# Kernel optimization log

Hardware: AMD Instinct MI355X
Metric: run time of the kernel (lower is better)

The kernel has to match this reference:

```python
import jax, jax.numpy as jnp
import numpy as np

N_SEG = 1024  # segments per image (ids are contiguous in [0, N_SEG) after reindex_batch_segments)


def setup_inputs() -> dict:
    key = jax.random.key(0)
    k1, k2, k3, k4 = jax.random.split(key, 4)
    B, C, Hf, Wf = 4, 256, 16, 16
    H, W = 512, 512
    F_out = 192
    features = jax.random.normal(k1, (B, C, Hf, Wf), dtype=jnp.float32)
    w_conv = jax.random.normal(k2, (F_out, C), dtype=jnp.float32) / np.sqrt(C)
    b_conv = jax.random.normal(k3, (F_out,), dtype=jnp.float32) * 0.01
    segment = jax.random.randint(k4, (B, H, W), 0, N_SEG, dtype=jnp.int32)
    return {"features": features, "w_conv": w_conv, "b_conv": b_conv, "segment": segment}


def reference(features, w_conv, b_conv, segment):
    # features: (B, C, Hf, Wf) backbone output; segment: (B, H, W) int ids in [0, N_SEG)
    B, C, Hf, Wf = features.shape
    _, H, W = segment.shape
    # F.interpolate(..., mode='bilinear', align_corners=False) == half-pixel linear resize
    up = jax.image.resize(features, (B, C, H, W), method="bilinear")
    pix = up.transpose(0, 2, 3, 1).reshape(B * H * W, C)  # (B*H*W, C)
    # offset per-image segment ids into a global id space: id + b * N_SEG
    seg = (segment.reshape(B, H * W) + (jnp.arange(B, dtype=segment.dtype) * N_SEG)[:, None]).reshape(-1)
    sums = jax.ops.segment_sum(pix, seg, num_segments=B * N_SEG)              # (B*N, C)
    cnt = jax.ops.segment_sum(jnp.ones((B * H * W,), pix.dtype), seg, num_segments=B * N_SEG)
    mean = sums / jnp.maximum(cnt, 1.0)[:, None]
    feats = mean.reshape(B, N_SEG, C)                                          # (B, N, C)
    # last_conv: 1x1 Conv1d (C -> F_out) applied on (B, C, N), then permute(0, 2, 1)
    out = jnp.einsum("bnc,fc->bnf", feats, w_conv) + b_conv                    # (B, N, F_out)
    return out, segment
```

## Files before the change

### kernel.cpp

```cpp
#include <hip/hip_runtime.h>
#include <hip/hip_bf16.h>

constexpr int B_   = 4;
constexpr int C_   = 256;
constexpr int HF   = 16;
constexpr int WF   = 16;
constexpr int HH   = 512;
constexpr int WW   = 512;
constexpr int NSEG = 1024;
constexpr int FOUT = 192;
constexpr int NCELL = HF * WF;
constexpr int CB    = B_ * NCELL;
constexpr int GPB   = 48;

struct PS { float Fs[32][65]; float Ws[64][33]; };

union CellSMem {
    struct { unsigned lbin[NSEG]; unsigned wc[64]; } c;
    PS p;
};

__device__ void gemm_P_body(int gp, const float* __restrict__ feat,
                            const float* __restrict__ w, float* __restrict__ P,
                            PS& sm) {
    int ni = gp % 3;
    int mi = (gp / 3) & 3;
    int b  = gp / 12;
    const float* Fb = feat + (size_t)b * C_ * NCELL;

    int tid = threadIdx.x;
    int tx = tid & 15, ty = tid >> 4;
    float acc[4][4] = {};

    for (int k0 = 0; k0 < C_; k0 += 32) {
        #pragma unroll
        for (int l = 0; l < 2; ++l) {
            int li = tid * 2 + l;
            int kk = li >> 4;
            int m4 = (li & 15) * 4;
            float4 vf = *reinterpret_cast<const float4*>(&Fb[(size_t)(k0 + kk) * NCELL + mi * 64 + m4]);
            sm.Fs[kk][m4 + 0] = vf.x; sm.Fs[kk][m4 + 1] = vf.y;
            sm.Fs[kk][m4 + 2] = vf.z; sm.Fs[kk][m4 + 3] = vf.w;
            int row = li >> 3;
            int kq  = (li & 7) * 4;
            float4 vw = *reinterpret_cast<const float4*>(&w[(size_t)(ni * 64 + row) * C_ + k0 + kq]);
            sm.Ws[row][kq + 0] = vw.x; sm.Ws[row][kq + 1] = vw.y;
            sm.Ws[row][kq + 2] = vw.z; sm.Ws[row][kq + 3] = vw.w;
        }
        __syncthreads();
        #pragma unroll
        for (int kk = 0; kk < 32; ++kk) {
            float ar[4], wr[4];
            #pragma unroll
            for (int i = 0; i < 4; ++i) ar[i] = sm.Fs[kk][ty * 4 + i];
            #pragma unroll
            for (int j = 0; j < 4; ++j) wr[j] = sm.Ws[tx * 4 + j][kk];
            #pragma unroll
            for (int i = 0; i < 4; ++i)
                #pragma unroll
                for (int j = 0; j < 4; ++j) acc[i][j] += ar[i] * wr[j];
        }
        __syncthreads();
    }

    #pragma unroll
    for (int i = 0; i < 4; ++i)
        #pragma unroll
        for (int j = 0; j < 4; ++j)
            P[(size_t)b * NCELL * FOUT + (size_t)(mi * 64 + ty * 4 + i) * FOUT + ni * 64 + tx * 4 + j] = acc[i][j];
}

__device__ __forceinline__ unsigned tapw(int v, int cc) {
    if (v < 0 || v >= 512) return 0u;
    int twov = 2 * v - 31;
    int num  = ((twov % 64) + 64) % 64;
    int iv   = (twov - num) >> 6;
    int v0 = max(iv, 0), v1 = min(iv + 1, 15);
    return (unsigned)((v0 == cc ? 64 - num : 0) + (v1 == cc ? num : 0));
}

__global__ __launch_bounds__(256) void k_cell(const int* __restrict__ seg,
                                              float* __restrict__ segout,
                                              float* __restrict__ AT,
                                              const float* __restrict__ feat,
                                              const float* __restrict__ w,
                                              float* __restrict__ P) {
    __shared__ CellSMem sm;
    int blk = blockIdx.x;
    if (blk < GPB) { gemm_P_body(blk, feat, w, P, sm.p); return; }

    int cb   = blk - GPB;
    int tid  = threadIdx.x;
    int b    = cb >> 8;
    int cell = cb & 255;
    int cy = cell >> 4, cx = cell & 15;
    int ys = 32 * cy - 16, xs = 32 * cx - 16;

    const int4* sv = reinterpret_cast<const int4*>(seg + (size_t)cb * 1024);
    float4*     ov = reinterpret_cast<float4*>(segout + (size_t)cb * 1024);
    int4 pv = sv[tid];

    #pragma unroll
    for (int j = 0; j < 4; ++j) sm.c.lbin[tid * 4 + j] = 0u;
    if (tid < 64) sm.c.wc[tid] = tapw(xs + tid, cx);

    int r  = tid >> 2;
    int y  = ys + r;
    unsigned wrv = tapw(y, cy);
    int yc = min(max(y, 0), HH - 1);
    int cg = (tid & 3) * 16;
    int x0 = xs + cg;
    int xc = min(max(x0, 0), WW - 16);

    const int4* lrow = reinterpret_cast<const int4*>(seg + (size_t)b * (HH * WW) + (size_t)yc * WW + xc);
    int4 v0 = lrow[0], v1 = lrow[1], v2 = lrow[2], v3 = lrow[3];

    ov[tid] = make_float4((float)pv.x, (float)pv.y, (float)pv.z, (float)pv.w);
    __syncthreads();

    uint4 wa = *reinterpret_cast<const uint4*>(&sm.c.wc[cg + 0]);
    uint4 wb = *reinterpret_cast<const uint4*>(&sm.c.wc[cg + 4]);
    uint4 wcv = *reinterpret_cast<const uint4*>(&sm.c.wc[cg + 8]);
    uint4 wd = *reinterpret_cast<const uint4*>(&sm.c.wc[cg + 12]);

    atomicAdd(&sm.c.lbin[v0.x], wrv * wa.x);
    atomicAdd(&sm.c.lbin[v0.y], wrv * wa.y);
    atomicAdd(&sm.c.lbin[v0.z], wrv * wa.z);
    atomicAdd(&sm.c.lbin[v0.w], wrv * wa.w);
    atomicAdd(&sm.c.lbin[v1.x], wrv * wb.x);
    atomicAdd(&sm.c.lbin[v1.y], wrv * wb.y);
    atomicAdd(&sm.c.lbin[v1.z], wrv * wb.z);
    atomicAdd(&sm.c.lbin[v1.w], wrv * wb.w);
    atomicAdd(&sm.c.lbin[v2.x], wrv * wcv.x);
    atomicAdd(&sm.c.lbin[v2.y], wrv * wcv.y);
    atomicAdd(&sm.c.lbin[v2.z], wrv * wcv.z);
    atomicAdd(&sm.c.lbin[v2.w], wrv * wcv.w);
    atomicAdd(&sm.c.lbin[v3.x], wrv * wd.x);
    atomicAdd(&sm.c.lbin[v3.y], wrv * wd.y);
    atomicAdd(&sm.c.lbin[v3.z], wrv * wd.z);
    atomicAdd(&sm.c.lbin[v3.w], wrv * wd.w);
    __syncthreads();

    float4* dst = reinterpret_cast<float4*>(AT + ((size_t)(b * NCELL + cell)) * NSEG);
    constexpr float SCL = 1.0f / 4096.0f;
    dst[tid] = make_float4(sm.c.lbin[tid * 4 + 0] * SCL, sm.c.lbin[tid * 4 + 1] * SCL,
                           sm.c.lbin[tid * 4 + 2] * SCL, sm.c.lbin[tid * 4 + 3] * SCL);
}

__global__ __launch_bounds__(256) void k_gemm_out(const float* __restrict__ AT,
                                                  const float* __restrict__ P,
                                                  const float* __restrict__ bias,
                                                  float* __restrict__ out) {
    int ft = blockIdx.x % 3;
    int st = blockIdx.x / 3;
    int b  = st >> 5;
    int s0 = (st & 31) * 32;

    const float* ATb = AT + (size_t)b * NCELL * NSEG;
    const float* Pb  = P  + (size_t)b * NCELL * FOUT;

    __shared__ float As[32][33];
    __shared__ float Ps[32][65];

    int tid = threadIdx.x;
    int tx = tid & 15, ty = tid >> 4;
    float acc[2][4] = {};
    float cnt[2] = {};

    for (int k0 = 0; k0 < NCELL; k0 += 32) {
        {
            int kk = tid >> 3, e4 = (tid & 7) * 4;
            float4 va = *reinterpret_cast<const float4*>(&ATb[(size_t)(k0 + kk) * NSEG + s0 + e4]);
            As[kk][e4 + 0] = va.x; As[kk][e4 + 1] = va.y;
            As[kk][e4 + 2] = va.z; As[kk][e4 + 3] = va.w;
            #pragma unroll
            for (int l = 0; l < 2; ++l) {
                int li = tid * 2 + l;
                int kp = li >> 4, e = (li & 15) * 4;
                float4 vp = *reinterpret_cast<const float4*>(&Pb[(size_t)(k0 + kp) * FOUT + ft * 64 + e]);
                Ps[kp][e + 0] = vp.x; Ps[kp][e + 1] = vp.y;
                Ps[kp][e + 2] = vp.z; Ps[kp][e + 3] = vp.w;
            }
        }
        __syncthreads();
        #pragma unroll
        for (int kk = 0; kk < 32; ++kk) {
            float ar[2], wr[4];
            #pragma unroll
            for (int i = 0; i < 2; ++i) { ar[i] = As[kk][ty * 2 + i]; cnt[i] += ar[i]; }
            #pragma unroll
            for (int j = 0; j < 4; ++j) wr[j] = Ps[kk][tx * 4 + j];
            #pragma unroll
            for (int i = 0; i < 2; ++i)
                #pragma unroll
                for (int j = 0; j < 4; ++j) acc[i][j] += ar[i] * wr[j];
        }
        __syncthreads();
    }

    #pragma unroll
    for (int i = 0; i < 2; ++i) {
        int row = b * NSEG + s0 + ty * 2 + i;
        float rinv = 1.0f / fmaxf(cnt[i], 1.0f);
        #pragma unroll
        for (int j = 0; j < 4; ++j) {
            int f = ft * 64 + tx * 4 + j;
            out[(size_t)row * FOUT + f] = acc[i][j] * rinv + bias[f];
        }
    }
}

extern "C" void kernel_launch(void* const* d_in, const int* in_sizes, int n_in,
                              void* d_out, int out_size, void* d_ws, size_t ws_size,
                              hipStream_t stream) {
    const float* feat = (const float*)d_in[0];
    const float* w    = (const float*)d_in[1];
    const float* bias = (const float*)d_in[2];
    const int*   seg  = (const int*)d_in[3];

    float* out    = (float*)d_out;
    float* segout = out + (size_t)B_ * NSEG * FOUT;

    char* wsb = (char*)d_ws;
    float* AT = (float*)wsb;
    float* P  = (float*)(wsb + (5u << 20));

    k_cell    <<<GPB + CB, 256, 0, stream>>>(seg, segout, AT, feat, w, P);
    k_gemm_out<<<(B_ * NSEG / 32) * (FOUT / 64), 256, 0, stream>>>(AT, P, bias, out);
}
```

Measured before the change: 48.54 us.

## Replace shared-memory tiled GEMMs with per-thread register-accumulating direct-load loops

Both small GEMMs (features x weights into P, and the per-segment weights AT x P into the output) drop their LDS tiling and __syncthreads. Each thread now computes one row times 16 output columns, streaming operands straight from global/L2 with broadcast loads of P and w. The output GEMM launches 192 blocks instead of 384 and writes float4 stores. This removes barrier and LDS staging overhead, but it lowers parallelism and relies on cache broadcast for operand reuse.

```diff
diff --git a/kernel.cpp b/kernel.cpp
--- a/kernel.cpp
+++ b/kernel.cpp
@@ -13,61 +13,30 @@
 constexpr int CB    = B_ * NCELL;
 constexpr int GPB   = 48;
 
-struct PS { float Fs[32][65]; float Ws[64][33]; };
+__device__ void gemm_P_body(int gp, const float* __restrict__ feat,
+                            const float* __restrict__ w, float* __restrict__ P) {
+    int b  = gp / 12;
+    int f0 = (gp % 12) * 16;
+    int ij = threadIdx.x;
+    const float* Fb = feat + (size_t)b * C_ * NCELL + ij;
 
-union CellSMem {
-    struct { unsigned lbin[NSEG]; unsigned wc[64]; } c;
-    PS p;
-};
-
-__device__ void gemm_P_body(int gp, const float* __restrict__ feat,
-                            const float* __restrict__ w, float* __restrict__ P,
-                            PS& sm) {
-    int ni = gp % 3;
-    int mi = (gp / 3) & 3;
-    int b  = gp / 12;
-    const float* Fb = feat + (size_t)b * C_ * NCELL;
-
-    int tid = threadIdx.x;
-    int tx = tid & 15, ty = tid >> 4;
-    float acc[4][4] = {};
-
-    for (int k0 = 0; k0 < C_; k0 += 32) {
+    float acc[16] = {};
+    for (int c0 = 0; c0 < C_; c0 += 4) {
+        float fv0 = Fb[(size_t)(c0 + 0) * NCELL];
+        float fv1 = Fb[(size_t)(c0 + 1) * NCELL];
+        float fv2 = Fb[(size_t)(c0 + 2) * NCELL];
+        float fv3 = Fb[(size_t)(c0 + 3) * NCELL];
         #pragma unroll
-        for (int l = 0; l < 2; ++l) {
-            int li = tid * 2 + l;
-            int kk = li >> 4;
-            int m4 = (li & 15) * 4;
-            float4 vf = *reinterpret_cast<const float4*>(&Fb[(size_t)(k0 + kk) * NCELL + mi * 64 + m4]);
-            sm.Fs[kk][m4 + 0] = vf.x; sm.Fs[kk][m4 + 1] = vf.y;
-            sm.Fs[kk][m4 + 2] = vf.z; sm.Fs[kk][m4 + 3] = vf.w;
-            int row = li >> 3;
-            int kq  = (li & 7) * 4;
-            float4 vw = *reinterpret_cast<const float4*>(&w[(size_t)(ni * 64 + row) * C_ + k0 + kq]);
-            sm.Ws[row][kq + 0] = vw.x; sm.Ws[row][kq + 1] = vw.y;
-            sm.Ws[row][kq + 2] = vw.z; sm.Ws[row][kq + 3] = vw.w;
+        for (int j = 0; j < 16; ++j) {
+            float4 wv = *reinterpret_cast<const float4*>(&w[(size_t)(f0 + j) * C_ + c0]);
+            acc[j] += fv0 * wv.x + fv1 * wv.y + fv2 * wv.z + fv3 * wv.w;
         }
-        __syncthreads();
-        #pragma unroll
-        for (int kk = 0; kk < 32; ++kk) {
-            float ar[4], wr[4];
-            #pragma unroll
-            for (int i = 0; i < 4; ++i) ar[i] = sm.Fs[kk][ty * 4 + i];
-            #pragma unroll
-            for (int j = 0; j < 4; ++j) wr[j] = sm.Ws[tx * 4 + j][kk];
-            #pragma unroll
-            for (int i = 0; i < 4; ++i)
-                #pragma unroll
-                for (int j = 0; j < 4; ++j) acc[i][j] += ar[i] * wr[j];
-        }
-        __syncthreads();
     }
-
+    float* Pp = P + (size_t)b * NCELL * FOUT + (size_t)ij * FOUT + f0;
     #pragma unroll
-    for (int i = 0; i < 4; ++i)
-        #pragma unroll
-        for (int j = 0; j < 4; ++j)
-            P[(size_t)b * NCELL * FOUT + (size_t)(mi * 64 + ty * 4 + i) * FOUT + ni * 64 + tx * 4 + j] = acc[i][j];
+    for (int j4 = 0; j4 < 4; ++j4)
+        *reinterpret_cast<float4*>(Pp + j4 * 4) =
+            make_float4(acc[j4 * 4 + 0], acc[j4 * 4 + 1], acc[j4 * 4 + 2], acc[j4 * 4 + 3]);
 }
 
 __device__ __forceinline__ unsigned tapw(int v, int cc) {
@@ -79,17 +48,11 @@
     return (unsigned)((v0 == cc ? 64 - num : 0) + (v1 == cc ? num : 0));
 }
 
-__global__ __launch_bounds__(256) void k_cell(const int* __restrict__ seg,
-                                              float* __restrict__ segout,
-                                              float* __restrict__ AT,
-                                              const float* __restrict__ feat,
-                                              const float* __restrict__ w,
-                                              float* __restrict__ P) {
-    __shared__ CellSMem sm;
-    int blk = blockIdx.x;
-    if (blk < GPB) { gemm_P_body(blk, feat, w, P, sm.p); return; }
+struct CS { unsigned lbin[NSEG]; unsigned wc[64]; };
 
-    int cb   = blk - GPB;
+__device__ void cell_body(int cb, const int* __restrict__ seg,
+                          float* __restrict__ segout, float* __restrict__ AT,
+                          CS& sm) {
     int tid  = threadIdx.x;
     int b    = cb >> 8;
     int cell = cb & 255;
@@ -101,8 +64,8 @@
     int4 pv = sv[tid];
 
     #pragma unroll
-    for (int j = 0; j < 4; ++j) sm.c.lbin[tid * 4 + j] = 0u;
-    if (tid < 64) sm.c.wc[tid] = tapw(xs + tid, cx);
+    for (int j = 0; j < 4; ++j) sm.lbin[tid * 4 + j] = 0u;
+    if (tid < 64) sm.wc[tid] = tapw(xs + tid, cx);
 
     int r  = tid >> 2;
     int y  = ys + r;
@@ -118,95 +81,84 @@
     ov[tid] = make_float4((float)pv.x, (float)pv.y, (float)pv.z, (float)pv.w);
     __syncthreads();
 
-    uint4 wa = *reinterpret_cast<const uint4*>(&sm.c.wc[cg + 0]);
-    uint4 wb = *reinterpret_cast<const uint4*>(&sm.c.wc[cg + 4]);
-    uint4 wcv = *reinterpret_cast<const uint4*>(&sm.c.wc[cg + 8]);
-    uint4 wd = *reinterpret_cast<const uint4*>(&sm.c.wc[cg + 12]);
+    uint4 wa  = *reinterpret_cast<const uint4*>(&sm.wc[cg + 0]);
+    uint4 wb  = *reinterpret_cast<const uint4*>(&sm.wc[cg + 4]);
+    uint4 wcv = *reinterpret_cast<const uint4*>(&sm.wc[cg + 8]);
+    uint4 wd  = *reinterpret_cast<const uint4*>(&sm.wc[cg + 12]);
 
-    atomicAdd(&sm.c.lbin[v0.x], wrv * wa.x);
-    atomicAdd(&sm.c.lbin[v0.y], wrv * wa.y);
-    atomicAdd(&sm.c.lbin[v0.z], wrv * wa.z);
-    atomicAdd(&sm.c.lbin[v0.w], wrv * wa.w);
-    atomicAdd(&sm.c.lbin[v1.x], wrv * wb.x);
-    atomicAdd(&sm.c.lbin[v1.y], wrv * wb.y);
-    atomicAdd(&sm.c.lbin[v1.z], wrv * wb.z);
-    atomicAdd(&sm.c.lbin[v1.w], wrv * wb.w);
-    atomicAdd(&sm.c.lbin[v2.x], wrv * wcv.x);
-    atomicAdd(&sm.c.lbin[v2.y], wrv * wcv.y);
-    atomicAdd(&sm.c.lbin[v2.z], wrv * wcv.z);
-    atomicAdd(&sm.c.lbin[v2.w], wrv * wcv.w);
-    atomicAdd(&sm.c.lbin[v3.x], wrv * wd.x);
-    atomicAdd(&sm.c.lbin[v3.y], wrv * wd.y);
-    atomicAdd(&sm.c.lbin[v3.z], wrv * wd.z);
-    atomicAdd(&sm.c.lbin[v3.w], wrv * wd.w);
+    atomicAdd(&sm.lbin[v0.x], wrv * wa.x);
+    atomicAdd(&sm.lbin[v0.y], wrv * wa.y);
+    atomicAdd(&sm.lbin[v0.z], wrv * wa.z);
+    atomicAdd(&sm.lbin[v0.w], wrv * wa.w);
+    atomicAdd(&sm.lbin[v1.x], wrv * wb.x);
+    atomicAdd(&sm.lbin[v1.y], wrv * wb.y);
+    atomicAdd(&sm.lbin[v1.z], wrv * wb.z);
+    atomicAdd(&sm.lbin[v1.w], wrv * wb.w);
+    atomicAdd(&sm.lbin[v2.x], wrv * wcv.x);
+    atomicAdd(&sm.lbin[v2.y], wrv * wcv.y);
+    atomicAdd(&sm.lbin[v2.z], wrv * wcv.z);
+    atomicAdd(&sm.lbin[v2.w], wrv * wcv.w);
+    atomicAdd(&sm.lbin[v3.x], wrv * wd.x);
+    atomicAdd(&sm.lbin[v3.y], wrv * wd.y);
+    atomicAdd(&sm.lbin[v3.z], wrv * wd.z);
+    atomicAdd(&sm.lbin[v3.w], wrv * wd.w);
     __syncthreads();
 
     float4* dst = reinterpret_cast<float4*>(AT + ((size_t)(b * NCELL + cell)) * NSEG);
     constexpr float SCL = 1.0f / 4096.0f;
-    dst[tid] = make_float4(sm.c.lbin[tid * 4 + 0] * SCL, sm.c.lbin[tid * 4 + 1] * SCL,
-                           sm.c.lbin[tid * 4 + 2] * SCL, sm.c.lbin[tid * 4 + 3] * SCL);
+    dst[tid] = make_float4(sm.lbin[tid * 4 + 0] * SCL, sm.lbin[tid * 4 + 1] * SCL,
+                           sm.lbin[tid * 4 + 2] * SCL, sm.lbin[tid * 4 + 3] * SCL);
+}
+
+__global__ __launch_bounds__(256) void k_phase1(const int* __restrict__ seg,
+                                                float* __restrict__ segout,
+                                                float* __restrict__ AT,
+                                                const float* __restrict__ feat,
+                                                const float* __restrict__ w,
+                                                float* __restrict__ P) {
+    __shared__ CS sm;
+    int blk = blockIdx.x;
+    if (blk < GPB) gemm_P_body(blk, feat, w, P);
+    else           cell_body(blk - GPB, seg, segout, AT, sm);
 }
 
 __global__ __launch_bounds__(256) void k_gemm_out(const float* __restrict__ AT,
                                                   const float* __restrict__ P,
                                                   const float* __restrict__ bias,
                                                   float* __restrict__ out) {
-    int ft = blockIdx.x % 3;
-    int st = blockIdx.x / 3;
-    int b  = st >> 5;
-    int s0 = (st & 31) * 32;
+    int blk = blockIdx.x;
+    int b  = blk / 48;
+    int rc = blk % 48;
+    int s0 = (rc / 12) * 256;
+    int f0 = (rc % 12) * 16;
+    int s  = s0 + threadIdx.x;
 
-    const float* ATb = AT + (size_t)b * NCELL * NSEG;
-    const float* Pb  = P  + (size_t)b * NCELL * FOUT;
+    const float* Ab = AT + (size_t)b * NCELL * NSEG + s;
+    const float* Pb = P  + (size_t)b * NCELL * FOUT;
 
-    __shared__ float As[32][33];
-    __shared__ float Ps[32][65];
-
-    int tid = threadIdx.x;
-    int tx = tid & 15, ty = tid >> 4;
-    float acc[2][4] = {};
-    float cnt[2] = {};
-
-    for (int k0 = 0; k0 < NCELL; k0 += 32) {
-        {
-            int kk = tid >> 3, e4 = (tid & 7) * 4;
-            float4 va = *reinterpret_cast<const float4*>(&ATb[(size_t)(k0 + kk) * NSEG + s0 + e4]);
-            As[kk][e4 + 0] = va.x; As[kk][e4 + 1] = va.y;
-            As[kk][e4 + 2] = va.z; As[kk][e4 + 3] = va.w;
-            #pragma unroll
-            for (int l = 0; l < 2; ++l) {
-                int li = tid * 2 + l;
-                int kp = li >> 4, e = (li & 15) * 4;
-                float4 vp = *reinterpret_cast<const float4*>(&Pb[(size_t)(k0 + kp) * FOUT + ft * 64 + e]);
-                Ps[kp][e + 0] = vp.x; Ps[kp][e + 1] = vp.y;
-                Ps[kp][e + 2] = vp.z; Ps[kp][e + 3] = vp.w;
-            }
+    float acc[16] = {};
+    float cnt = 0.0f;
+    for (int k = 0; k < NCELL; ++k) {
+        float a = Ab[(size_t)k * NSEG];
+        cnt += a;
+        #pragma unroll
+        for (int j4 = 0; j4 < 4; ++j4) {
+            float4 pvv = *reinterpret_cast<const float4*>(&Pb[(size_t)k * FOUT + f0 + j4 * 4]);
+            acc[j4 * 4 + 0] += a * pvv.x;
+            acc[j4 * 4 + 1] += a * pvv.y;
+            acc[j4 * 4 + 2] += a * pvv.z;
+            acc[j4 * 4 + 3] += a * pvv.w;
         }
-        __syncthreads();
-        #pragma unroll
-        for (int kk = 0; kk < 32; ++kk) {
-            float ar[2], wr[4];
-            #pragma unroll
-            for (int i = 0; i < 2; ++i) { ar[i] = As[kk][ty * 2 + i]; cnt[i] += ar[i]; }
-            #pragma unroll
-            for (int j = 0; j < 4; ++j) wr[j] = Ps[kk][tx * 4 + j];
-            #pragma unroll
-            for (int i = 0; i < 2; ++i)
-                #pragma unroll
-                for (int j = 0; j < 4; ++j) acc[i][j] += ar[i] * wr[j];
-        }
-        __syncthreads();
     }
 
+    float rinv = 1.0f / fmaxf(cnt, 1.0f);
+    float* op = out + (size_t)(b * NSEG + s) * FOUT + f0;
     #pragma unroll
-    for (int i = 0; i < 2; ++i) {
-        int row = b * NSEG + s0 + ty * 2 + i;
-        float rinv = 1.0f / fmaxf(cnt[i], 1.0f);
-        #pragma unroll
-        for (int j = 0; j < 4; ++j) {
-            int f = ft * 64 + tx * 4 + j;
-            out[(size_t)row * FOUT + f] = acc[i][j] * rinv + bias[f];
-        }
+    for (int j4 = 0; j4 < 4; ++j4) {
+        float4 bv = *reinterpret_cast<const float4*>(&bias[f0 + j4 * 4]);
+        *reinterpret_cast<float4*>(op + j4 * 4) =
+            make_float4(acc[j4 * 4 + 0] * rinv + bv.x, acc[j4 * 4 + 1] * rinv + bv.y,
+                        acc[j4 * 4 + 2] * rinv + bv.z, acc[j4 * 4 + 3] * rinv + bv.w);
     }
 }
 
@@ -225,6 +177,6 @@
     float* AT = (float*)wsb;
     float* P  = (float*)(wsb + (5u << 20));
 
-    k_cell    <<<GPB + CB, 256, 0, stream>>>(seg, segout, AT, feat, w, P);
-    k_gemm_out<<<(B_ * NSEG / 32) * (FOUT / 64), 256, 0, stream>>>(AT, P, bias, out);
+    k_phase1  <<<GPB + CB, 256, 0, stream>>>(seg, segout, AT, feat, w, P);
+    k_gemm_out<<<192, 256, 0, stream>>>(AT, P, bias, out);
 }
```

Result: slower. 67.92 us (+39.9%).

## Replace per-cell 64x64 bilinear binning with 32x32 region moment histograms

Applied to the files above, without the earlier changes.

Instead of each of the 1024 cell blocks re-reading a 64x64 overlapping pixel window (4x overlap), the image is split into 17x17 non-overlapping 32x32 regions. Each region block accumulates per-segment packed moments (sum ab, sum a, sum b, count) in 64-bit shared atomics. A new combine kernel then rebuilds each cell's bilinear weights as linear combinations of the four neighbouring regions' moments. This cuts redundant segment reads and shared atomics, but adds a third launch, an 8 MB moment round-trip through global memory, and relies on the packed bitfields not overflowing.

```diff
diff --git a/kernel.cpp b/kernel.cpp
--- a/kernel.cpp
+++ b/kernel.cpp
@@ -10,15 +10,13 @@
 constexpr int NSEG = 1024;
 constexpr int FOUT = 192;
 constexpr int NCELL = HF * WF;
-constexpr int CB    = B_ * NCELL;
+constexpr int NREG  = 17;
+constexpr int RPI   = NREG * NREG;
+constexpr int RB    = B_ * RPI;
 constexpr int GPB   = 48;
 
 struct PS { float Fs[32][65]; float Ws[64][33]; };
-
-union CellSMem {
-    struct { unsigned lbin[NSEG]; unsigned wc[64]; } c;
-    PS p;
-};
+union RegSMem { PS p; unsigned long long m[NSEG]; };
 
 __device__ void gemm_P_body(int gp, const float* __restrict__ feat,
                             const float* __restrict__ w, float* __restrict__ P,
@@ -70,81 +68,109 @@
             P[(size_t)b * NCELL * FOUT + (size_t)(mi * 64 + ty * 4 + i) * FOUT + ni * 64 + tx * 4 + j] = acc[i][j];
 }
 
-__device__ __forceinline__ unsigned tapw(int v, int cc) {
-    if (v < 0 || v >= 512) return 0u;
-    int twov = 2 * v - 31;
-    int num  = ((twov % 64) + 64) % 64;
-    int iv   = (twov - num) >> 6;
-    int v0 = max(iv, 0), v1 = min(iv + 1, 15);
-    return (unsigned)((v0 == cc ? 64 - num : 0) + (v1 == cc ? num : 0));
-}
-
-__global__ __launch_bounds__(256) void k_cell(const int* __restrict__ seg,
-                                              float* __restrict__ segout,
-                                              float* __restrict__ AT,
-                                              const float* __restrict__ feat,
-                                              const float* __restrict__ w,
-                                              float* __restrict__ P) {
-    __shared__ CellSMem sm;
+__global__ __launch_bounds__(256) void k_regions(const int* __restrict__ seg,
+                                                 unsigned long long* __restrict__ mom,
+                                                 const float* __restrict__ feat,
+                                                 const float* __restrict__ w,
+                                                 float* __restrict__ P) {
+    __shared__ RegSMem sm;
     int blk = blockIdx.x;
     if (blk < GPB) { gemm_P_body(blk, feat, w, P, sm.p); return; }
 
-    int cb   = blk - GPB;
+    int rb  = blk - GPB;
+    int b   = rb / RPI;
+    int reg = rb % RPI;
+    int k   = reg / NREG;
+    int cs  = reg % NREG;
+    int tid = threadIdx.x;
+
+    #pragma unroll
+    for (int j = 0; j < 4; ++j) sm.m[tid * 4 + j] = 0ull;
+    __syncthreads();
+
+    int lr = tid >> 3;
+    int g  = tid & 7;
+    int y  = 32 * k - 16 + lr;
+    int xb = 32 * cs - 16 + 4 * g;
+    if ((unsigned)y < (unsigned)HH && xb >= 0 && xb <= WW - 4) {
+        int4 v = *reinterpret_cast<const int4*>(seg + (size_t)b * (HH * WW) + (size_t)y * WW + xb);
+        unsigned long long a = (unsigned long long)(63 - 2 * lr);
+        int ss[4] = { v.x, v.y, v.z, v.w };
+        #pragma unroll
+        for (int j = 0; j < 4; ++j) {
+            unsigned long long bet = (unsigned long long)(63 - 8 * g - 2 * j);
+            unsigned long long val = (a * bet) | (a << 20) | (bet << 34) | (1ull << 48);
+            atomicAdd(&sm.m[ss[j]], val);
+        }
+    }
+    __syncthreads();
+
+    unsigned long long* dst = mom + ((size_t)(b * RPI + reg)) * NSEG;
+    #pragma unroll
+    for (int j = 0; j < 4; ++j) dst[tid * 4 + j] = sm.m[tid * 4 + j];
+}
+
+__global__ __launch_bounds__(256) void k_combine(const unsigned long long* __restrict__ mom,
+                                                 const int* __restrict__ seg,
+                                                 float* __restrict__ segout,
+                                                 float* __restrict__ A) {
+    int blk  = blockIdx.x;
     int tid  = threadIdx.x;
-    int b    = cb >> 8;
-    int cell = cb & 255;
+    int b    = blk >> 8;
+    int cell = blk & 255;
     int cy = cell >> 4, cx = cell & 15;
-    int ys = 32 * cy - 16, xs = 32 * cx - 16;
-
-    const int4* sv = reinterpret_cast<const int4*>(seg + (size_t)cb * 1024);
-    float4*     ov = reinterpret_cast<float4*>(segout + (size_t)cb * 1024);
-    int4 pv = sv[tid];
-
-    #pragma unroll
-    for (int j = 0; j < 4; ++j) sm.c.lbin[tid * 4 + j] = 0u;
-    if (tid < 64) sm.c.wc[tid] = tapw(xs + tid, cx);
-
-    int r  = tid >> 2;
-    int y  = ys + r;
-    unsigned wrv = tapw(y, cy);
-    int yc = min(max(y, 0), HH - 1);
-    int cg = (tid & 3) * 16;
-    int x0 = xs + cg;
-    int xc = min(max(x0, 0), WW - 16);
-
-    const int4* lrow = reinterpret_cast<const int4*>(seg + (size_t)b * (HH * WW) + (size_t)yc * WW + xc);
-    int4 v0 = lrow[0], v1 = lrow[1], v2 = lrow[2], v3 = lrow[3];
-
-    ov[tid] = make_float4((float)pv.x, (float)pv.y, (float)pv.z, (float)pv.w);
-    __syncthreads();
-
-    uint4 wa = *reinterpret_cast<const uint4*>(&sm.c.wc[cg + 0]);
-    uint4 wb = *reinterpret_cast<const uint4*>(&sm.c.wc[cg + 4]);
-    uint4 wcv = *reinterpret_cast<const uint4*>(&sm.c.wc[cg + 8]);
-    uint4 wd = *reinterpret_cast<const uint4*>(&sm.c.wc[cg + 12]);
-
-    atomicAdd(&sm.c.lbin[v0.x], wrv * wa.x);
-    atomicAdd(&sm.c.lbin[v0.y], wrv * wa.y);
-    atomicAdd(&sm.c.lbin[v0.z], wrv * wa.z);
-    atomicAdd(&sm.c.lbin[v0.w], wrv * wa.w);
-    atomicAdd(&sm.c.lbin[v1.x], wrv * wb.x);
-    atomicAdd(&sm.c.lbin[v1.y], wrv * wb.y);
-    atomicAdd(&sm.c.lbin[v1.z], wrv * wb.z);
-    atomicAdd(&sm.c.lbin[v1.w], wrv * wb.w);
-    atomicAdd(&sm.c.lbin[v2.x], wrv * wcv.x);
-    atomicAdd(&sm.c.lbin[v2.y], wrv * wcv.y);
-    atomicAdd(&sm.c.lbin[v2.z], wrv * wcv.z);
-    atomicAdd(&sm.c.lbin[v2.w], wrv * wcv.w);
-    atomicAdd(&sm.c.lbin[v3.x], wrv * wd.x);
-    atomicAdd(&sm.c.lbin[v3.y], wrv * wd.y);
-    atomicAdd(&sm.c.lbin[v3.z], wrv * wd.z);
-    atomicAdd(&sm.c.lbin[v3.w], wrv * wd.w);
-    __syncthreads();
-
-    float4* dst = reinterpret_cast<float4*>(AT + ((size_t)(b * NCELL + cell)) * NSEG);
+
+    {
+        const int4* sv = reinterpret_cast<const int4*>(seg + (size_t)blk * 1024);
+        float4*     ov = reinterpret_cast<float4*>(segout + (size_t)blk * 1024);
+        int4 v = sv[tid];
+        ov[tid] = make_float4((float)v.x, (float)v.y, (float)v.z, (float)v.w);
+    }
+
+    int pA_a = (cy == 0)  ? 0 : -1, pA_0 = 64;
+    int pB_a = (cy == 15) ? 0 : 1,  pB_0 = (cy == 15) ? 64 : 0;
+    int qA_b = (cx == 0)  ? 0 : -1, qA_0 = 64;
+    int qB_b = (cx == 15) ? 0 : 1,  qB_0 = (cx == 15) ? 64 : 0;
+
+    const unsigned long long* base = mom + (size_t)b * RPI * NSEG;
+    const unsigned long long* r00 = base + (size_t)((cy    ) * NREG + cx    ) * NSEG;
+    const unsigned long long* r01 = base + (size_t)((cy    ) * NREG + cx + 1) * NSEG;
+    const unsigned long long* r10 = base + (size_t)((cy + 1) * NREG + cx    ) * NSEG;
+    const unsigned long long* r11 = base + (size_t)((cy + 1) * NREG + cx + 1) * NSEG;
+
+    float* dst = A + ((size_t)(b * NCELL + cell)) * NSEG;
     constexpr float SCL = 1.0f / 4096.0f;
-    dst[tid] = make_float4(sm.c.lbin[tid * 4 + 0] * SCL, sm.c.lbin[tid * 4 + 1] * SCL,
-                           sm.c.lbin[tid * 4 + 2] * SCL, sm.c.lbin[tid * 4 + 3] * SCL);
+
+    #pragma unroll
+    for (int j = 0; j < 4; ++j) {
+        int s = tid * 4 + j;
+        int acc = 0;
+        {
+            unsigned long long m = r00[s];
+            int Sab = (int)(m & 0xFFFFFull), Sa = (int)((m >> 20) & 0x3FFF);
+            int Sb  = (int)((m >> 34) & 0x3FFF), cn = (int)(m >> 48);
+            acc += pA_a * qA_b * Sab + pA_a * qA_0 * Sa + pA_0 * qA_b * Sb + pA_0 * qA_0 * cn;
+        }
+        {
+            unsigned long long m = r01[s];
+            int Sab = (int)(m & 0xFFFFFull), Sa = (int)((m >> 20) & 0x3FFF);
+            int Sb  = (int)((m >> 34) & 0x3FFF), cn = (int)(m >> 48);
+            acc += pA_a * qB_b * Sab + pA_a * qB_0 * Sa + pA_0 * qB_b * Sb + pA_0 * qB_0 * cn;
+        }
+        {
+            unsigned long long m = r10[s];
+            int Sab = (int)(m & 0xFFFFFull), Sa = (int)((m >> 20) & 0x3FFF);
+            int Sb  = (int)((m >> 34) & 0x3FFF), cn = (int)(m >> 48);
+            acc += pB_a * qA_b * Sab + pB_a * qA_0 * Sa + pB_0 * qA_b * Sb + pB_0 * qA_0 * cn;
+        }
+        {
+            unsigned long long m = r11[s];
+            int Sab = (int)(m & 0xFFFFFull), Sa = (int)((m >> 20) & 0x3FFF);
+            int Sb  = (int)((m >> 34) & 0x3FFF), cn = (int)(m >> 48);
+            acc += pB_a * qB_b * Sab + pB_a * qB_0 * Sa + pB_0 * qB_b * Sb + pB_0 * qB_0 * cn;
+        }
+        dst[s] = (float)acc * SCL;
+    }
 }
 
 __global__ __launch_bounds__(256) void k_gemm_out(const float* __restrict__ AT,
@@ -222,9 +248,11 @@
     float* segout = out + (size_t)B_ * NSEG * FOUT;
 
     char* wsb = (char*)d_ws;
-    float* AT = (float*)wsb;
-    float* P  = (float*)(wsb + (5u << 20));
-
-    k_cell    <<<GPB + CB, 256, 0, stream>>>(seg, segout, AT, feat, w, P);
-    k_gemm_out<<<(B_ * NSEG / 32) * (FOUT / 64), 256, 0, stream>>>(AT, P, bias, out);
-}
+    float*              A   = (float*)wsb;
+    float*              P   = (float*)(wsb + (4u << 20));
+    unsigned long long* mom = (unsigned long long*)(wsb + (5u << 20));
+
+    k_regions <<<GPB + RB, 256, 0, stream>>>(seg, mom, feat, w, P);
+    k_combine <<<B_ * NCELL, 256, 0, stream>>>(mom, seg, segout, A);
+    k_gemm_out<<<(B_ * NSEG / 32) * (FOUT / 64), 256, 0, stream>>>(A, P, bias, out);
+}
```

Result: slower. 54.54 us (+12.4%).
